# Performance work log

Hardware: AMD Instinct MI355X
Metric: run time of the kernel (lower is better)

Reference implementation:

```python
import jax, jax.numpy as jnp
import numpy as np

D_MODEL = 768
MLP_DIM = 3072
N_EXPERTS = 8
TOP_K = 2
GROUP_DET = 1024
GROUP_CLS = 128


def _route(x, wr, k, capacity):
    """Deterministic top-k softmax router with capacity (vmoe-style).

    x: [G, S, d], wr: [d, E]. Returns dispatch [G,S,E,C] (0/1) and
    combine [G,S,E,C] (gate-weighted).
    """
    G, S, _ = x.shape
    E = wr.shape[1]
    gates = jax.nn.softmax(jnp.einsum('gsd,de->gse', x, wr))  # [G,S,E]
    gval, gidx = jax.lax.top_k(gates, k)                      # [G,S,k]
    # rank-major ordering: all rank-0 choices first, then rank-1, ...
    idx = jnp.swapaxes(gidx, 1, 2).reshape(G, k * S)          # [G,kS]
    val = jnp.swapaxes(gval, 1, 2).reshape(G, k * S)
    oh = jax.nn.one_hot(idx, E, dtype=x.dtype)                # [G,kS,E]
    # position of each assignment in its expert's buffer
    pos = jnp.take_along_axis(jnp.cumsum(oh, axis=1), idx[..., None], axis=2)[..., 0] - 1.0
    keep = (pos < capacity).astype(x.dtype)                   # drop overflow tokens
    posc = jnp.where(pos < capacity, pos, 0.0).astype(jnp.int32)
    slot = jax.nn.one_hot(posc, capacity, dtype=x.dtype)      # [G,kS,C]
    disp = oh[:, :, :, None] * slot[:, :, None, :] * keep[:, :, None, None]  # [G,kS,E,C]
    disp = disp.reshape(G, k, S, E, capacity)
    combine = (disp * val.reshape(G, k, S, 1, 1)).sum(axis=1)  # [G,S,E,C]
    dispatch = disp.sum(axis=1)                                # [G,S,E,C]
    return dispatch, combine


def _expert_mlp(xe, w1, b1, w2, b2):
    # xe: [E,G,C,d]; per-expert params w1:[E,d,m], b1:[E,m], w2:[E,m,d], b2:[E,d]
    h = jax.nn.gelu(jnp.einsum('egcd,edm->egcm', xe, w1) + b1[:, None, None, :])
    return jnp.einsum('egcm,emd->egcd', h, w2) + b2[:, None, None, :]


def _moe_stream(x3, group_size, wr, w1, b1, w2, b2):
    B, S, d = x3.shape
    x = x3.reshape(-1, group_size, d)                         # [G,gs,d]
    capacity = group_size * TOP_K // N_EXPERTS
    dispatch, combine = _route(x, wr, TOP_K, capacity)
    xe = jnp.einsum('gsec,gsd->egcd', dispatch, x)            # gather to experts
    ye = _expert_mlp(xe, w1, b1, w2, b2)                      # grouped MLP
    y = jnp.einsum('gsec,egcd->gsd', combine, ye)             # weighted scatter back
    return y.reshape(B, S, d)


def setup_inputs() -> dict:
    key = jax.random.key(0)
    ks = jax.random.split(key, 8)
    xav1 = float(np.sqrt(6.0 / (D_MODEL + MLP_DIM)))
    xavr = float(np.sqrt(6.0 / (D_MODEL + N_EXPERTS)))
    return {
        'inputs_det': jax.random.normal(ks[0], (8, 1024, D_MODEL), jnp.float32),
        'inputs_cls': jax.random.normal(ks[1], (8, 128, D_MODEL), jnp.float32),
        'wr_det': jax.random.uniform(ks[2], (D_MODEL, N_EXPERTS), jnp.float32, -xavr, xavr),
        'wr_cls': jax.random.uniform(ks[3], (D_MODEL, N_EXPERTS), jnp.float32, -xavr, xavr),
        'w1': jax.random.uniform(ks[4], (N_EXPERTS, D_MODEL, MLP_DIM), jnp.float32, -xav1, xav1),
        'b1': jax.random.normal(ks[5], (N_EXPERTS, MLP_DIM), jnp.float32) * 1e-6,
        'w2': jax.random.uniform(ks[6], (N_EXPERTS, MLP_DIM, D_MODEL), jnp.float32, -xav1, xav1),
        'b2': jax.random.normal(ks[7], (N_EXPERTS, D_MODEL), jnp.float32) * 1e-6,
    }


def reference(inputs_det, inputs_cls, wr_det, wr_cls, w1, b1, w2, b2):
    out_det = _moe_stream(inputs_det, GROUP_DET, wr_det, w1, b1, w2, b2)
    out_cls = _moe_stream(inputs_cls, GROUP_CLS, wr_cls, w1, b1, w2, b2)
    return (out_det, out_cls)
```

## Files before the change

kernel.cpp:

```cpp
#include <hip/hip_runtime.h>
#include <hip/hip_bf16.h>
#include <math.h>

typedef __bf16 bf16;
typedef __bf16 bf16x8 __attribute__((ext_vector_type(8)));
typedef __bf16 bf16x4 __attribute__((ext_vector_type(4)));
typedef float  f32x4  __attribute__((ext_vector_type(4)));

#define D_MODEL 768
#define MLP_DIM 3072

#define SZ_W1T   ((size_t)8*3072*768*2)
#define SZ_W2T   ((size_t)8*768*3072*2)
#define SZ_XED   ((size_t)8*8*256*768*2)
#define SZ_XEC   ((size_t)8*8*32*768*2)
#define SZ_HD    ((size_t)8*2048*3072*2)
#define SZ_HC    ((size_t)8*256*3072*2)
#define SZ_YED   ((size_t)8*2048*768*2)
#define SZ_YEC   ((size_t)8*256*768*2)
#define SZ_RID   ((size_t)8192*8)
#define SZ_RGD   ((size_t)8192*8)
#define SZ_RIC   ((size_t)1024*8)
#define SZ_RGC   ((size_t)1024*8)
#define SZ_STD   ((size_t)8*8*256*4)
#define SZ_STC   ((size_t)8*8*32*4)
#define SZ_TSD   ((size_t)2*8192*4)
#define SZ_TSC   ((size_t)2*1024*4)

#define OFF_W1T  ((size_t)0)
#define OFF_W2T  (OFF_W1T + SZ_W1T)
#define OFF_XED  (OFF_W2T + SZ_W2T)
#define OFF_XEC  (OFF_XED + SZ_XED)
#define OFF_HD   (OFF_XEC + SZ_XEC)
#define OFF_HC   (OFF_HD  + SZ_HD)
#define OFF_YED  (OFF_HC  + SZ_HC)
#define OFF_YEC  (OFF_YED + SZ_YED)
#define OFF_RID  (OFF_YEC + SZ_YEC)
#define OFF_RGD  (OFF_RID + SZ_RID)
#define OFF_RIC  (OFF_RGD + SZ_RGD)
#define OFF_RGC  (OFF_RIC + SZ_RIC)
#define OFF_STD  (OFF_RGC + SZ_RGC)
#define OFF_STC  (OFF_STD + SZ_STD)
#define OFF_TSD  (OFF_STC + SZ_STC)
#define OFF_TSC  (OFF_TSD + SZ_TSD)

__device__ __forceinline__ void lds_load16(const void* g, void* l) {
  __builtin_amdgcn_global_load_lds((__attribute__((address_space(1))) void*)g,
                                   (__attribute__((address_space(3))) void*)l,
                                   16, 0, 0);
}

__device__ __forceinline__ float gelu_fast(float x) {
  float x2 = x * x;
  float z = x * __builtin_fmaf(-0.07135481627f, x2, -1.5957691216f);
  float e = __expf(z);
  return x * __builtin_amdgcn_rcpf(1.f + e);
}

__device__ __forceinline__ void transpose64(const float* __restrict__ src,
                                            bf16* __restrict__ dst,
                                            int K, int N, int e, int t, float* tile) {
  int tiles_x = N >> 6;
  int ky = t / tiles_x;
  int n0 = (t - ky * tiles_x) * 64, k0 = ky * 64;
  const float* S_ = src + (size_t)e * K * N;
  bf16* D_ = dst + (size_t)e * K * N;
  int tid = threadIdx.x;
  int tx = tid & 15, ty = tid >> 4;
#pragma unroll
  for (int i = 0; i < 4; ++i) {
    float4 v = *(const float4*)(S_ + (size_t)(k0 + ty + i * 16) * N + (n0 + tx * 4));
    int r = ty + i * 16, c = tx * 4;
    tile[r * 65 + c] = v.x; tile[r * 65 + c + 1] = v.y;
    tile[r * 65 + c + 2] = v.z; tile[r * 65 + c + 3] = v.w;
  }
  __syncthreads();
  int n = tid >> 2, kq = (tid & 3) * 16;
  bf16 o[16];
#pragma unroll
  for (int j = 0; j < 16; ++j) o[j] = (bf16)tile[(kq + j) * 65 + n];
  bf16* drow = D_ + (size_t)(n0 + n) * K + (k0 + kq);
  *(bf16x8*)drow       = *(const bf16x8*)o;
  *(bf16x8*)(drow + 8) = *(const bf16x8*)(o + 8);
}

__global__ void router_kernel(const float* __restrict__ xd, const float* __restrict__ wrd,
                              const float* __restrict__ xc, const float* __restrict__ wrc,
                              int2* __restrict__ rid, float2* __restrict__ rgd,
                              int2* __restrict__ ric, float2* __restrict__ rgc,
                              int splitd) {
  int bid = blockIdx.x;
  const float *x, *wr; int2* ridx; float2* rgate;
  if (bid < splitd) { x = xd; wr = wrd; ridx = rid; rgate = rgd; }
  else { bid -= splitd; x = xc; wr = wrc; ridx = ric; rgate = rgc; }
  int wave = threadIdx.x >> 6;
  int lane = threadIdx.x & 63;
  int t = bid * 4 + wave;
  const float* xr = x + (size_t)t * D_MODEL;
  float acc[8];
#pragma unroll
  for (int e = 0; e < 8; ++e) acc[e] = 0.f;
  for (int d = lane; d < D_MODEL; d += 64) {
    float xv = xr[d];
    const float* w = wr + d * 8;
    float4 a = *(const float4*)w;
    float4 b = *(const float4*)(w + 4);
    acc[0] += xv * a.x; acc[1] += xv * a.y; acc[2] += xv * a.z; acc[3] += xv * a.w;
    acc[4] += xv * b.x; acc[5] += xv * b.y; acc[6] += xv * b.z; acc[7] += xv * b.w;
  }
#pragma unroll
  for (int off = 32; off > 0; off >>= 1) {
#pragma unroll
    for (int e = 0; e < 8; ++e) acc[e] += __shfl_xor(acc[e], off, 64);
  }
  float mx = acc[0];
#pragma unroll
  for (int e = 1; e < 8; ++e) mx = fmaxf(mx, acc[e]);
  float p[8]; float z = 0.f;
#pragma unroll
  for (int e = 0; e < 8; ++e) { p[e] = __expf(acc[e] - mx); z += p[e]; }
  int i1 = 0;
#pragma unroll
  for (int e = 1; e < 8; ++e) if (p[e] > p[i1]) i1 = e;
  int i2 = (i1 == 0) ? 1 : 0;
#pragma unroll
  for (int e = 0; e < 8; ++e) if (e != i1 && p[e] > p[i2]) i2 = e;
  if (lane == 0) {
    float inv = 1.f / z;
    ridx[t]  = make_int2(i1, i2);
    rgate[t] = make_float2(p[i1] * inv, p[i2] * inv);
  }
}

__global__ void positions_kernel(const int2* __restrict__ rid, int* __restrict__ std_,
                                 int* __restrict__ tsd_, const int2* __restrict__ ric,
                                 int* __restrict__ stc_, int* __restrict__ tsc_) {
  __shared__ int2 sh[1024];
  int bid = blockIdx.x;
  const int2* ridx; int *slot_token, *tok_slot; int S, C, g;
  if (bid < 8) { ridx = rid; slot_token = std_; tok_slot = tsd_; S = 1024; C = 256; g = bid; }
  else { ridx = ric; slot_token = stc_; tok_slot = tsc_; S = 128; C = 32; g = bid - 8; }
  int lane = threadIdx.x;
  int ntok = 8 * S;
  for (int i = lane; i < S; i += 64) sh[i] = ridx[g * S + i];
  __builtin_amdgcn_s_waitcnt(0);
  unsigned long long ltmask = (1ull << lane) - 1ull;
  int cnt[8];
#pragma unroll
  for (int e = 0; e < 8; ++e) cnt[e] = 0;
  int nch = (2 * S) >> 6;
  for (int ch = 0; ch < nch; ++ch) {
    int a = (ch << 6) + lane;
    int r = (a >= S) ? 1 : 0;
    int s = a - r * S;
    int2 id = sh[s];
    int  e  = r ? id.y : id.x;
    unsigned long long mymask = 0;
    int add[8];
#pragma unroll
    for (int ee = 0; ee < 8; ++ee) {
      unsigned long long mk = __ballot(e == ee);
      if (e == ee) mymask = mk;
      add[ee] = __popcll(mk);
    }
    int pos = cnt[e] + __popcll(mymask & ltmask);
    int sl = (e * 8 + g) * C + pos;
    if (pos < C) slot_token[sl] = s;
    tok_slot[r * ntok + g * S + s] = (pos < C) ? sl : -1;
#pragma unroll
    for (int ee = 0; ee < 8; ++ee) cnt[ee] += add[ee];
  }
#pragma unroll
  for (int e = 0; e < 8; ++e) {
    for (int i = cnt[e] + lane; i < C; i += 64)
      slot_token[(e * 8 + g) * C + i] = -1;
  }
}

__global__ void gather_w1t_kernel(const float* __restrict__ xd, const int* __restrict__ std_,
                                  bf16* __restrict__ xed, const float* __restrict__ xc,
                                  const int* __restrict__ stc_, bf16* __restrict__ xec,
                                  int splitd, const float* __restrict__ w1,
                                  bf16* __restrict__ w1t, int nT) {
  __shared__ float tile[64 * 65];
  int bid = blockIdx.x;
  if (bid < nT) {
    int e = bid / 576;
    int t = bid - e * 576;
    transpose64(w1, w1t, 768, 3072, e, t, tile);
    return;
  }
  bid -= nT;
  const float* x; const int* slot_token; bf16* xe; int S, C;
  if (bid < splitd) { x = xd; slot_token = std_; xe = xed; S = 1024; C = 256; }
  else { bid -= splitd; x = xc; slot_token = stc_; xe = xec; S = 128; C = 32; }
  int slot = bid * 4 + (threadIdx.x >> 6);
  int lane = threadIdx.x & 63;
  int g = (slot / C) & 7;
  int s = slot_token[slot];
  bf16* dst = xe + (size_t)slot * D_MODEL;
  const float* xr = x + ((size_t)g * S + (s < 0 ? 0 : s)) * D_MODEL;
#pragma unroll
  for (int j = 0; j < 3; ++j) {
    int idx = j * 256 + lane * 4;
    float4 v;
    if (s >= 0) v = *(const float4*)(xr + idx);
    else        v = make_float4(0.f, 0.f, 0.f, 0.f);
    bf16 o[4] = {(bf16)v.x, (bf16)v.y, (bf16)v.z, (bf16)v.w};
    *(uint2*)(dst + idx) = *(const uint2*)o;
  }
}

__global__ void combine_kernel(const int* __restrict__ tsd_, const float2* __restrict__ rgd,
                               const bf16* __restrict__ yed, float* __restrict__ outd,
                               const int* __restrict__ tsc_, const float2* __restrict__ rgc,
                               const bf16* __restrict__ yec, float* __restrict__ outc,
                               int splitd) {
  int bid = blockIdx.x;
  const int* tok_slot; const float2* rgate; const bf16* ye; float* out; int ntok;
  if (bid < splitd) { tok_slot = tsd_; rgate = rgd; ye = yed; out = outd; ntok = 8192; }
  else { bid -= splitd; tok_slot = tsc_; rgate = rgc; ye = yec; out = outc; ntok = 1024; }
  int t = bid * 4 + (threadIdx.x >> 6);
  int lane = threadIdx.x & 63;
  int s1 = tok_slot[t];
  int s2 = tok_slot[ntok + t];
  float2 gg = rgate[t];
  float g1 = (s1 < 0) ? 0.f : gg.x;
  float g2 = (s2 < 0) ? 0.f : gg.y;
  const bf16* y1 = ye + (size_t)(s1 < 0 ? 0 : s1) * D_MODEL;
  const bf16* y2 = ye + (size_t)(s2 < 0 ? 0 : s2) * D_MODEL;
  float* orow = out + (size_t)t * D_MODEL;
#pragma unroll
  for (int j = 0; j < 3; ++j) {
    int idx = j * 256 + lane * 4;
    bf16x4 a = *(const bf16x4*)(y1 + idx);
    bf16x4 b = *(const bf16x4*)(y2 + idx);
    float4 o;
    o.x = g1 * (float)a[0] + g2 * (float)b[0];
    o.y = g1 * (float)a[1] + g2 * (float)b[1];
    o.z = g1 * (float)a[2] + g2 * (float)b[2];
    o.w = g1 * (float)a[3] + g2 * (float)b[3];
    *(float4*)(orow + idx) = o;
  }
}

template <int GELU>
__launch_bounds__(256, 3)
__global__ void gemm_mfma(const bf16* __restrict__ Adet, const bf16* __restrict__ Acls,
                          const bf16* __restrict__ Btall, const float* __restrict__ biasall,
                          int Mdet, int Mcls, int N, int K,
                          int Nmd, int Nmc, int Nn, int minner, int splitd,
                          bf16* __restrict__ Odet, bf16* __restrict__ Ocls,
                          const float* __restrict__ tsrc, bf16* __restrict__ tdst,
                          int nGemm) {
  __shared__ __align__(16) bf16 smem[16384];

  int bid = blockIdx.x;
  if (bid >= nGemm) {
    int t2 = bid - nGemm;
    int e = t2 / 576;
    int t = t2 - e * 576;
    transpose64(tsrc, tdst, 3072, 768, e, t, (float*)smem);
    return;
  }

  const bf16* Aall; bf16* Oall; int M, Nm;
  if (bid < splitd) { Aall = Adet; Oall = Odet; M = Mdet; Nm = Nmd; }
  else { bid -= splitd; Aall = Acls; Oall = Ocls; M = Mcls; Nm = Nmc; }
  const int e   = bid & 7;
  const int seq = bid >> 3;
  int m_t, n_t;
  if (minner) { n_t = seq / Nm; m_t = seq - n_t * Nm; }
  else        { m_t = seq / Nn; n_t = seq - m_t * Nn; }
  const int n0 = n_t * 128;
  const int m0 = m_t * 128;
  const int tid  = threadIdx.x;
  const int wave = tid >> 6, lane = tid & 63;
  const int wm = (wave >> 1) * 64, wn = (wave & 1) * 64;
  const int lrow = lane & 15, lquad = lane >> 4;

  bf16* As = smem;
  bf16* Bs = smem + 8192;

  const bf16* A  = Aall  + (size_t)e * M * K;
  const bf16* Bt = Btall + (size_t)e * N * K;

  const int srow = tid >> 3;
  const int gq   = (tid & 7) ^ (srow & 7);
  const bf16* Asrc = A  + (size_t)(m0 + srow) * K + gq * 8;
  const bf16* Bsrc = Bt + (size_t)(n0 + srow) * K + gq * 8;
  char* AsB = (char*)As;
  char* BsB = (char*)Bs;
  const int ldsw = wave * 1024;

  const float* bias = biasall + (size_t)e * N;
  float bfr[4];
#pragma unroll
  for (int ni = 0; ni < 4; ++ni) bfr[ni] = bias[n0 + wn + ni * 16 + lrow];

  f32x4 acc[4][4];
#pragma unroll
  for (int mi = 0; mi < 4; ++mi)
#pragma unroll
    for (int ni = 0; ni < 4; ++ni) acc[mi][ni] = {0.f, 0.f, 0.f, 0.f};

  const int xsw = lrow & 7;
  const int nsteps = K >> 6;
  for (int kt = 0; kt < nsteps; ++kt) {
    const bf16* a0 = Asrc + kt * 64;
    const bf16* b0 = Bsrc + kt * 64;
#pragma unroll
    for (int rd = 0; rd < 4; ++rd) {
      lds_load16(a0 + (size_t)(rd * 32) * K, AsB + rd * 4096 + ldsw);
      lds_load16(b0 + (size_t)(rd * 32) * K, BsB + rd * 4096 + ldsw);
    }
    __syncthreads();
#pragma unroll
    for (int h = 0; h < 2; ++h) {
      bf16x8 fa[4], fb[4];
      const int ca = ((h * 4 + lquad) ^ xsw) * 8;
#pragma unroll
      for (int i = 0; i < 4; ++i) {
        fa[i] = *(const bf16x8*)(As + (wm + i * 16 + lrow) * 64 + ca);
        fb[i] = *(const bf16x8*)(Bs + (wn + i * 16 + lrow) * 64 + ca);
      }
#pragma unroll
      for (int mi = 0; mi < 4; ++mi)
#pragma unroll
        for (int ni = 0; ni < 4; ++ni)
          acc[mi][ni] = __builtin_amdgcn_mfma_f32_16x16x32_bf16(fa[mi], fb[ni], acc[mi][ni], 0, 0, 0);
    }
    __syncthreads();
  }

#pragma unroll
  for (int mi = 0; mi < 4; ++mi) {
#pragma unroll
    for (int r = 0; r < 4; ++r) {
      int row = wm + mi * 16 + lquad * 4 + r;
#pragma unroll
      for (int ni = 0; ni < 4; ++ni) {
        int colL = wn + ni * 16 + lrow;
        float v = acc[mi][ni][r] + bfr[ni];
        if (GELU) v = gelu_fast(v);
        int chunk = (colL >> 3) ^ (row & 7);
        smem[row * 128 + chunk * 8 + (colL & 7)] = (bf16)v;
      }
    }
  }
  __syncthreads();
  bf16* O = Oall + (size_t)e * M * N;
#pragma unroll
  for (int it = 0; it < 8; ++it) {
    int idx = it * 256 + tid;
    int row = idx >> 4;
    int ck  = idx & 15;
    int pchunk = ck ^ (row & 7);
    bf16x8 vv = *(const bf16x8*)(smem + row * 128 + pchunk * 8);
    *(bf16x8*)(O + (size_t)(m0 + row) * N + n0 + ck * 8) = vv;
  }
}

template <int GELU>
__launch_bounds__(512, 2)
__global__ void gemm_mfma8p(const bf16* __restrict__ Adet, const bf16* __restrict__ Acls,
                            const bf16* __restrict__ Btall, const float* __restrict__ biasall,
                            int Mdet, int Mcls, int N, int K,
                            int Nmd, int Nmc, int Nn, int minner, int splitd,
                            bf16* __restrict__ Odet, bf16* __restrict__ Ocls) {
  int bid = blockIdx.x;
  const bf16* Aall; bf16* Oall; int M, Nm;
  if (bid < splitd) { Aall = Adet; Oall = Odet; M = Mdet; Nm = Nmd; }
  else { bid -= splitd; Aall = Acls; Oall = Ocls; M = Mcls; Nm = Nmc; }
  const int e   = bid & 7;
  const int seq = bid >> 3;
  int m_t, n_t;
  if (minner) { n_t = seq / Nm; m_t = seq - n_t * Nm; }
  else        { m_t = seq / Nn; n_t = seq - m_t * Nn; }
  const int n0 = n_t * 256;
  const int m0 = m_t * 256;
  const int tid  = threadIdx.x;
  const int wave = tid >> 6, lane = tid & 63;
  const int wm = (wave >> 2) * 128, wn = (wave & 3) * 64;
  const int lrow = lane & 15, lquad = lane >> 4;

  __shared__ __align__(16) bf16 smem[65536];
  char* smemB = (char*)smem;

  const bf16* A  = Aall  + (size_t)e * M * K;
  const bf16* Bt = Btall + (size_t)e * N * K;

  const int srow0 = tid >> 3;
  const int gq    = (tid & 7) ^ (srow0 & 7);
  const bf16* Asrc = A  + (size_t)(m0 + srow0) * K + gq * 8;
  const bf16* Bsrc = Bt + (size_t)(n0 + srow0) * K + gq * 8;
  const int ldsw = wave * 1024;

  const int aBase = (wm ? 8192 : 0) + lrow * 64;
  const int bBase = 16384 + (wn >= 128 ? 8192 : 0) + (wn & 64) * 64 + lrow * 64;
  const int ca0 = (lquad ^ (lrow & 7)) * 8;
  const int ca1 = ca0 ^ 32;

  const float* bias = biasall + (size_t)e * N;
  float bfr[4];
#pragma unroll
  for (int ni = 0; ni < 4; ++ni) bfr[ni] = bias[n0 + wn + ni * 16 + lrow];

  f32x4 acc[8][4];
#pragma unroll
  for (int mi = 0; mi < 8; ++mi)
#pragma unroll
    for (int ni = 0; ni < 4; ++ni) acc[mi][ni] = {0.f, 0.f, 0.f, 0.f};

  bf16x8 fa[2][4], fb0[2][2], fb1[2][2];

#define STG_A(buf, half, kt) do { \
    const bf16* _s = Asrc + (size_t)((half) * 128) * K + (size_t)(kt) * 64; \
    char* _d = smemB + (buf) * 65536 + (half) * 16384 + ldsw; \
    lds_load16(_s, _d); \
    lds_load16(_s + (size_t)64 * K, _d + 8192); \
  } while (0)
#define STG_B(buf, half, kt) do { \
    const bf16* _s = Bsrc + (size_t)((half) * 128) * K + (size_t)(kt) * 64; \
    char* _d = smemB + (buf) * 65536 + 32768 + (half) * 16384 + ldsw; \
    lds_load16(_s, _d); \
    lds_load16(_s + (size_t)64 * K, _d + 8192); \
  } while (0)
#define LDA(buf, qm) do { \
    const bf16* _p = smem + (buf) * 32768 + aBase + (qm) * 4096; \
    _Pragma("unroll") \
    for (int _i = 0; _i < 4; ++_i) { \
      fa[0][_i] = *(const bf16x8*)(_p + _i * 1024 + ca0); \
      fa[1][_i] = *(const bf16x8*)(_p + _i * 1024 + ca1); \
    } \
  } while (0)
#define LDB(buf, qn, FB) do { \
    const bf16* _p = smem + (buf) * 32768 + bBase + (qn) * 2048; \
    _Pragma("unroll") \
    for (int _j = 0; _j < 2; ++_j) { \
      FB[0][_j] = *(const bf16x8*)(_p + _j * 1024 + ca0); \
      FB[1][_j] = *(const bf16x8*)(_p + _j * 1024 + ca1); \
    } \
  } while (0)
#define MM(qm, qn, FB) do { \
    __builtin_amdgcn_s_setprio(1); \
    _Pragma("unroll") \
    for (int _h = 0; _h < 2; ++_h) \
      _Pragma("unroll") \
      for (int _i = 0; _i < 4; ++_i) \
        _Pragma("unroll") \
        for (int _j = 0; _j < 2; ++_j) \
          acc[(qm) * 4 + _i][(qn) * 2 + _j] = __builtin_amdgcn_mfma_f32_16x16x32_bf16( \
              fa[_h][_i], FB[_h][_j], acc[(qm) * 4 + _i][(qn) * 2 + _j], 0, 0, 0); \
    __builtin_amdgcn_s_setprio(0); \
  } while (0)
#define BAR() __builtin_amdgcn_s_barrier()
#define VMC4() asm volatile("s_waitcnt vmcnt(4)" ::: "memory")

  const int nt = K >> 6;
  const int niter = nt >> 1;

  STG_B(0, 0, 0); STG_B(0, 1, 0); STG_A(0, 0, 0); STG_A(0, 1, 0);
  STG_B(1, 0, 1); STG_B(1, 1, 1);
  VMC4();
  BAR();

  for (int it = 0; it < niter; ++it) {
    const int k1 = 2 * it + 1;
    const int k2 = (2 * it + 2 < nt) ? 2 * it + 2 : nt - 1;
    const int k3 = (2 * it + 3 < nt) ? 2 * it + 3 : nt - 1;
    LDA(0, 0); LDB(0, 0, fb0); STG_A(1, 0, k1); BAR(); MM(0, 0, fb0); BAR();
    LDB(0, 1, fb1);            STG_A(1, 1, k1); BAR(); MM(0, 1, fb1); BAR();
    LDA(0, 1);                 STG_B(0, 0, k2); BAR(); MM(1, 1, fb1); BAR();
                               STG_B(0, 1, k2); VMC4();
                                                BAR(); MM(1, 0, fb0); BAR();
    LDA(1, 0); LDB(1, 0, fb0); STG_A(0, 0, k2); BAR(); MM(0, 0, fb0); BAR();
    LDB(1, 1, fb1);            STG_A(0, 1, k2); BAR(); MM(0, 1, fb1); BAR();
    LDA(1, 1);                 STG_B(1, 0, k3); BAR(); MM(1, 1, fb1); BAR();
                               STG_B(1, 1, k3); VMC4();
                                                BAR(); MM(1, 0, fb0); BAR();
  }

#undef STG_A
#undef STG_B
#undef LDA
#undef LDB
#undef MM
#undef BAR
#undef VMC4

  __syncthreads();
#pragma unroll
  for (int mi = 0; mi < 8; ++mi) {
#pragma unroll
    for (int r = 0; r < 4; ++r) {
      int row = wm + mi * 16 + lquad * 4 + r;
#pragma unroll
      for (int ni = 0; ni < 4; ++ni) {
        int colL = wn + ni * 16 + lrow;
        float v = acc[mi][ni][r] + bfr[ni];
        if (GELU) v = gelu_fast(v);
        int chunk = (colL >> 3) ^ (row & 7);
        smem[row * 256 + chunk * 8 + (colL & 7)] = (bf16)v;
      }
    }
  }
  __syncthreads();
  bf16* O = Oall + (size_t)e * M * N;
#pragma unroll
  for (int itw = 0; itw < 16; ++itw) {
    int idx = itw * 512 + tid;
    int row = idx >> 5;
    int ck  = idx & 31;
    int pchunk = ck ^ (row & 7);
    bf16x8 vv = *(const bf16x8*)(smem + row * 256 + pchunk * 8);
    *(bf16x8*)(O + (size_t)(m0 + row) * N + n0 + ck * 8) = vv;
  }
}

extern "C" void kernel_launch(void* const* d_in, const int* in_sizes, int n_in,
                              void* d_out, int out_size, void* d_ws, size_t ws_size,
                              hipStream_t stream) {
  (void)in_sizes; (void)n_in; (void)ws_size; (void)out_size;
  const float* x_det  = (const float*)d_in[0];
  const float* x_cls  = (const float*)d_in[1];
  const float* wr_det = (const float*)d_in[2];
  const float* wr_cls = (const float*)d_in[3];
  const float* w1     = (const float*)d_in[4];
  const float* b1     = (const float*)d_in[5];
  const float* w2     = (const float*)d_in[6];
  const float* b2     = (const float*)d_in[7];
  float* out = (float*)d_out;
  char*  ws  = (char*)d_ws;

  bf16*   w1t    = (bf16*)(ws + OFF_W1T);
  bf16*   w2t    = (bf16*)(ws + OFF_W2T);
  bf16*   xe_det = (bf16*)(ws + OFF_XED);
  bf16*   xe_cls = (bf16*)(ws + OFF_XEC);
  bf16*   h_det  = (bf16*)(ws + OFF_HD);
  bf16*   h_cls  = (bf16*)(ws + OFF_HC);
  bf16*   ye_det = (bf16*)(ws + OFF_YED);
  bf16*   ye_cls = (bf16*)(ws + OFF_YEC);
  int2*   ri_det = (int2*)(ws + OFF_RID);
  float2* rg_det = (float2*)(ws + OFF_RGD);
  int2*   ri_cls = (int2*)(ws + OFF_RIC);
  float2* rg_cls = (float2*)(ws + OFF_RGC);
  int*    st_det = (int*)(ws + OFF_STD);
  int*    st_cls = (int*)(ws + OFF_STC);
  int*    ts_det = (int*)(ws + OFF_TSD);
  int*    ts_cls = (int*)(ws + OFF_TSC);

  router_kernel<<<2048 + 256, 256, 0, stream>>>(x_det, wr_det, x_cls, wr_cls,
                                                ri_det, rg_det, ri_cls, rg_cls, 2048);

  positions_kernel<<<16, 64, 0, stream>>>(ri_det, st_det, ts_det, ri_cls, st_cls, ts_cls);

  gather_w1t_kernel<<<4608 + 4096 + 512, 256, 0, stream>>>(
      x_det, st_det, xe_det, x_cls, st_cls, xe_cls, 4096, w1, w1t, 4608);

  gemm_mfma<1><<<8 * 16 * 24 + 8 * 2 * 24 + 4608, 256, 0, stream>>>(
      xe_det, xe_cls, w1t, b1, 2048, 256, 3072, 768,
      16, 2, 24, 1, 8 * 16 * 24, h_det, h_cls, w2, w2t, 3456);

  gemm_mfma8p<0><<<8 * 8 * 3 + 8 * 1 * 3, 512, 0, stream>>>(
      h_det, h_cls, w2t, b2, 2048, 256, 768, 3072,
      8, 1, 3, 0, 8 * 8 * 3, ye_det, ye_cls);

  combine_kernel<<<2048 + 256, 256, 0, stream>>>(ts_det, rg_det, ye_det, out,
                                                 ts_cls, rg_cls, ye_cls,
                                                 out + (size_t)8192 * 768, 2048);
}
```

Baseline: 421.2 us.

## Fuse w1 transpose into router and merge positions with token gather

The w1 transpose blocks move into the router launch. The positions computation is merged with the token gather: each gather block recomputes its group's slot assignment into shared memory and then gathers rows, which removes one launch and the slot_token global array. The work is redundant, since the ballot-based scan runs 64 times per det group. That serial single-wave scan now sits at the start of every gather block, adding latency before the gather can begin.

```diff
diff --git a/kernel.cpp b/kernel.cpp
--- a/kernel.cpp
+++ b/kernel.cpp
@@ -84,15 +84,23 @@
   *(bf16x8*)(drow + 8) = *(const bf16x8*)(o + 8);
 }
 
-__global__ void router_kernel(const float* __restrict__ xd, const float* __restrict__ wrd,
-                              const float* __restrict__ xc, const float* __restrict__ wrc,
-                              int2* __restrict__ rid, float2* __restrict__ rgd,
-                              int2* __restrict__ ric, float2* __restrict__ rgc,
-                              int splitd) {
+__global__ void router_w1t_kernel(const float* __restrict__ w1, bf16* __restrict__ w1t,
+                                  const float* __restrict__ xd, const float* __restrict__ wrd,
+                                  const float* __restrict__ xc, const float* __restrict__ wrc,
+                                  int2* __restrict__ rid, float2* __restrict__ rgd,
+                                  int2* __restrict__ ric, float2* __restrict__ rgc) {
+  __shared__ float tile[64 * 65];
   int bid = blockIdx.x;
+  if (bid < 4608) {
+    int e = bid / 576;
+    int t = bid - e * 576;
+    transpose64(w1, w1t, 768, 3072, e, t, tile);
+    return;
+  }
+  bid -= 4608;
   const float *x, *wr; int2* ridx; float2* rgate;
-  if (bid < splitd) { x = xd; wr = wrd; ridx = rid; rgate = rgd; }
-  else { bid -= splitd; x = xc; wr = wrc; ridx = ric; rgate = rgc; }
+  if (bid < 2048) { x = xd; wr = wrd; ridx = rid; rgate = rgd; }
+  else { bid -= 2048; x = xc; wr = wrc; ridx = ric; rgate = rgc; }
   int wave = threadIdx.x >> 6;
   int lane = threadIdx.x & 63;
   int t = bid * 4 + wave;
@@ -132,82 +140,96 @@
   }
 }
 
-__global__ void positions_kernel(const int2* __restrict__ rid, int* __restrict__ std_,
-                                 int* __restrict__ tsd_, const int2* __restrict__ ric,
-                                 int* __restrict__ stc_, int* __restrict__ tsc_) {
+__global__ void posgather_kernel(const int2* __restrict__ rid, int* __restrict__ tsd_,
+                                 const float* __restrict__ xd, bf16* __restrict__ xed,
+                                 const int2* __restrict__ ric, int* __restrict__ tsc_,
+                                 const float* __restrict__ xc, bf16* __restrict__ xec) {
   __shared__ int2 sh[1024];
+  __shared__ int map[2048];
   int bid = blockIdx.x;
-  const int2* ridx; int *slot_token, *tok_slot; int S, C, g;
-  if (bid < 8) { ridx = rid; slot_token = std_; tok_slot = tsd_; S = 1024; C = 256; g = bid; }
-  else { ridx = ric; slot_token = stc_; tok_slot = tsc_; S = 128; C = 32; g = bid - 8; }
-  int lane = threadIdx.x;
-  int ntok = 8 * S;
-  for (int i = lane; i < S; i += 64) sh[i] = ridx[g * S + i];
-  __builtin_amdgcn_s_waitcnt(0);
-  unsigned long long ltmask = (1ull << lane) - 1ull;
-  int cnt[8];
-#pragma unroll
-  for (int e = 0; e < 8; ++e) cnt[e] = 0;
-  int nch = (2 * S) >> 6;
-  for (int ch = 0; ch < nch; ++ch) {
-    int a = (ch << 6) + lane;
-    int r = (a >= S) ? 1 : 0;
-    int s = a - r * S;
-    int2 id = sh[s];
-    int  e  = r ? id.y : id.x;
-    unsigned long long mymask = 0;
-    int add[8];
-#pragma unroll
-    for (int ee = 0; ee < 8; ++ee) {
-      unsigned long long mk = __ballot(e == ee);
-      if (e == ee) mymask = mk;
-      add[ee] = __popcll(mk);
-    }
-    int pos = cnt[e] + __popcll(mymask & ltmask);
-    int sl = (e * 8 + g) * C + pos;
-    if (pos < C) slot_token[sl] = s;
-    tok_slot[r * ntok + g * S + s] = (pos < C) ? sl : -1;
-#pragma unroll
-    for (int ee = 0; ee < 8; ++ee) cnt[ee] += add[ee];
-  }
-#pragma unroll
-  for (int e = 0; e < 8; ++e) {
-    for (int i = cnt[e] + lane; i < C; i += 64)
-      slot_token[(e * 8 + g) * C + i] = -1;
-  }
-}
-
-__global__ void gather_w1t_kernel(const float* __restrict__ xd, const int* __restrict__ std_,
-                                  bf16* __restrict__ xed, const float* __restrict__ xc,
-                                  const int* __restrict__ stc_, bf16* __restrict__ xec,
-                                  int splitd, const float* __restrict__ w1,
-                                  bf16* __restrict__ w1t, int nT) {
-  __shared__ float tile[64 * 65];
-  int bid = blockIdx.x;
-  if (bid < nT) {
-    int e = bid / 576;
-    int t = bid - e * 576;
-    transpose64(w1, w1t, 768, 3072, e, t, tile);
-    return;
-  }
-  bid -= nT;
-  const float* x; const int* slot_token; bf16* xe; int S, C;
-  if (bid < splitd) { x = xd; slot_token = std_; xe = xed; S = 1024; C = 256; }
-  else { bid -= splitd; x = xc; slot_token = stc_; xe = xec; S = 128; C = 32; }
-  int slot = bid * 4 + (threadIdx.x >> 6);
-  int lane = threadIdx.x & 63;
-  int g = (slot / C) & 7;
-  int s = slot_token[slot];
-  bf16* dst = xe + (size_t)slot * D_MODEL;
-  const float* xr = x + ((size_t)g * S + (s < 0 ? 0 : s)) * D_MODEL;
-#pragma unroll
-  for (int j = 0; j < 3; ++j) {
-    int idx = j * 256 + lane * 4;
-    float4 v;
-    if (s >= 0) v = *(const float4*)(xr + idx);
-    else        v = make_float4(0.f, 0.f, 0.f, 0.f);
-    bf16 o[4] = {(bf16)v.x, (bf16)v.y, (bf16)v.z, (bf16)v.w};
-    *(uint2*)(dst + idx) = *(const uint2*)o;
+  const int2* ridx; int* tok_slot; const float* x; bf16* xe;
+  int S, C, g, b, first;
+  if (bid < 512) {
+    ridx = rid; tok_slot = tsd_; x = xd; xe = xed;
+    S = 1024; C = 256; g = bid >> 6; b = bid & 63; first = (b == 0);
+  } else {
+    ridx = ric; tok_slot = tsc_; x = xc; xe = xec;
+    S = 128; C = 32; g = (bid - 512) >> 2; b = (bid - 512) & 3; first = (b == 0);
+  }
+  int tid = threadIdx.x;
+  for (int i = tid; i < 8 * C; i += 256) map[i] = -1;
+  if (tid < 64) {
+    for (int i = tid; i < S; i += 64) sh[i] = ridx[g * S + i];
+  }
+  __syncthreads();
+  if (tid < 64) {
+    int lane = tid;
+    int ntok = 8 * S;
+    __builtin_amdgcn_s_waitcnt(0);
+    unsigned long long ltmask = (1ull << lane) - 1ull;
+    int cnt[8];
+#pragma unroll
+    for (int e = 0; e < 8; ++e) cnt[e] = 0;
+    int nch = (2 * S) >> 6;
+    for (int ch = 0; ch < nch; ++ch) {
+      int a = (ch << 6) + lane;
+      int r = (a >= S) ? 1 : 0;
+      int s = a - r * S;
+      int2 id = sh[s];
+      int  e  = r ? id.y : id.x;
+      unsigned long long mymask = 0;
+      int add[8];
+#pragma unroll
+      for (int ee = 0; ee < 8; ++ee) {
+        unsigned long long mk = __ballot(e == ee);
+        if (e == ee) mymask = mk;
+        add[ee] = __popcll(mk);
+      }
+      int pos = cnt[e] + __popcll(mymask & ltmask);
+      if (pos < C) map[e * C + pos] = s;
+      if (first) tok_slot[r * ntok + g * S + s] = (pos < C) ? (e * 8 + g) * C + pos : -1;
+#pragma unroll
+      for (int ee = 0; ee < 8; ++ee) cnt[ee] += add[ee];
+    }
+  }
+  __syncthreads();
+  int wave = tid >> 6, lane = tid & 63;
+  if (bid < 512) {
+    int e = b >> 3, pos0 = (b & 7) * 32;
+#pragma unroll
+    for (int k = 0; k < 8; ++k) {
+      int pos = pos0 + wave * 8 + k;
+      int s = map[e * 256 + pos];
+      bf16* dst = xe + (size_t)((e * 8 + g) * 256 + pos) * D_MODEL;
+      const float* xr = x + ((size_t)g * 1024 + (s < 0 ? 0 : s)) * D_MODEL;
+#pragma unroll
+      for (int j = 0; j < 3; ++j) {
+        int idx = j * 256 + lane * 4;
+        float4 v;
+        if (s >= 0) v = *(const float4*)(xr + idx);
+        else        v = make_float4(0.f, 0.f, 0.f, 0.f);
+        bf16 o[4] = {(bf16)v.x, (bf16)v.y, (bf16)v.z, (bf16)v.w};
+        *(uint2*)(dst + idx) = *(const uint2*)o;
+      }
+    }
+  } else {
+#pragma unroll
+    for (int k = 0; k < 16; ++k) {
+      int idx64 = b * 64 + wave * 16 + k;
+      int e = idx64 >> 5, pos = idx64 & 31;
+      int s = map[e * 32 + pos];
+      bf16* dst = xe + (size_t)((e * 8 + g) * 32 + pos) * D_MODEL;
+      const float* xr = x + ((size_t)g * 128 + (s < 0 ? 0 : s)) * D_MODEL;
+#pragma unroll
+      for (int j = 0; j < 3; ++j) {
+        int idx = j * 256 + lane * 4;
+        float4 v;
+        if (s >= 0) v = *(const float4*)(xr + idx);
+        else        v = make_float4(0.f, 0.f, 0.f, 0.f);
+        bf16 o[4] = {(bf16)v.x, (bf16)v.y, (bf16)v.z, (bf16)v.w};
+        *(uint2*)(dst + idx) = *(const uint2*)o;
+      }
+    }
   }
 }
 
@@ -545,18 +567,15 @@
   float2* rg_det = (float2*)(ws + OFF_RGD);
   int2*   ri_cls = (int2*)(ws + OFF_RIC);
   float2* rg_cls = (float2*)(ws + OFF_RGC);
-  int*    st_det = (int*)(ws + OFF_STD);
-  int*    st_cls = (int*)(ws + OFF_STC);
   int*    ts_det = (int*)(ws + OFF_TSD);
   int*    ts_cls = (int*)(ws + OFF_TSC);
 
-  router_kernel<<<2048 + 256, 256, 0, stream>>>(x_det, wr_det, x_cls, wr_cls,
-                                                ri_det, rg_det, ri_cls, rg_cls, 2048);
-
-  positions_kernel<<<16, 64, 0, stream>>>(ri_det, st_det, ts_det, ri_cls, st_cls, ts_cls);
-
-  gather_w1t_kernel<<<4608 + 4096 + 512, 256, 0, stream>>>(
-      x_det, st_det, xe_det, x_cls, st_cls, xe_cls, 4096, w1, w1t, 4608);
+  router_w1t_kernel<<<4608 + 2048 + 256, 256, 0, stream>>>(
+      w1, w1t, x_det, wr_det, x_cls, wr_cls,
+      ri_det, rg_det, ri_cls, rg_cls);
+
+  posgather_kernel<<<512 + 32, 256, 0, stream>>>(
+      ri_det, ts_det, x_det, xe_det, ri_cls, ts_cls, x_cls, xe_cls);
 
   gemm_mfma<1><<<8 * 16 * 24 + 8 * 2 * 24 + 4608, 256, 0, stream>>>(
       xe_det, xe_cls, w1t, b1, 2048, 256, 3072, 768,
```

Result: no change. 425.1 us (+0.9%).
